# Kernel optimization log

Hardware: AMD Instinct MI355X
Metric: run time of the kernel (lower is better)

Reference implementation:

```python
import jax, jax.numpy as jnp
import numpy as np

N_NODES = 100000
N_EDGES = 1600000
IN_FEATS = 128
N_HIDDEN = 128
N_CLASSES = 40
EPS = 1e-12  # torch F.normalize eps


def _sage_conv(h, src, dst, W_self, b_self, W_neigh, b_neigh, act, norm):
    # mean aggregation over in-neighbors: dst receives from src
    agg = jax.ops.segment_sum(h[src], dst, num_segments=N_NODES)  # [N, D]
    deg = jax.ops.segment_sum(jnp.ones(dst.shape, h.dtype), dst, num_segments=N_NODES)
    h_neigh = agg / jnp.maximum(deg, 1.0)[:, None]
    out = h @ W_self + b_self + h_neigh @ W_neigh + b_neigh
    if act:
        out = jax.nn.relu(out)
    if norm:
        out = out / jnp.maximum(
            jnp.linalg.norm(out, axis=1, keepdims=True), EPS)
    return out


def setup_inputs() -> dict:
    key = jax.random.key(0)
    ks = jax.random.split(key, 16)
    def lin(k, fan_in, fan_out):
        s = 1.0 / np.sqrt(fan_in)
        return jax.random.uniform(k, (fan_in, fan_out), jnp.float32, -s, s)
    inp = {
        "features": jax.random.normal(ks[0], (N_NODES, IN_FEATS), jnp.float32),
        "src": jax.random.randint(ks[1], (N_EDGES,), 0, N_NODES, jnp.int32),
        "dst": jax.random.randint(ks[2], (N_EDGES,), 0, N_NODES, jnp.int32),
        # layer 0: in -> hidden
        "Ws0": lin(ks[3], IN_FEATS, N_HIDDEN), "bs0": jnp.zeros((N_HIDDEN,), jnp.float32),
        "Wn0": lin(ks[4], IN_FEATS, N_HIDDEN), "bn0": jnp.zeros((N_HIDDEN,), jnp.float32),
        # layer 1: hidden -> hidden
        "Ws1": lin(ks[5], N_HIDDEN, N_HIDDEN), "bs1": jnp.zeros((N_HIDDEN,), jnp.float32),
        "Wn1": lin(ks[6], N_HIDDEN, N_HIDDEN), "bn1": jnp.zeros((N_HIDDEN,), jnp.float32),
        # layer 2: hidden -> classes (no activation, no norm)
        "Ws2": lin(ks[7], N_HIDDEN, N_CLASSES), "bs2": jnp.zeros((N_CLASSES,), jnp.float32),
        "Wn2": lin(ks[8], N_HIDDEN, N_CLASSES), "bn2": jnp.zeros((N_CLASSES,), jnp.float32),
    }
    return inp


def reference(features, src, dst,
              Ws0, bs0, Wn0, bn0,
              Ws1, bs1, Wn1, bn1,
              Ws2, bs2, Wn2, bn2):
    h = _sage_conv(features, src, dst, Ws0, bs0, Wn0, bn0, act=True, norm=True)
    h = _sage_conv(h, src, dst, Ws1, bs1, Wn1, bn1, act=True, norm=True)
    out = _sage_conv(h, src, dst, Ws2, bs2, Wn2, bn2, act=False, norm=False)
    return out
```

## Files before the change

kernel.cpp:

```cpp
#include <hip/hip_runtime.h>
#include <hip/hip_bf16.h>

#define N_NODES_C 100000
#define N_EDGES_C 1600000
#define N_BUCK ((N_NODES_C + 255) / 256)
#define BCAP 4608
#define PART_NB 160
#define PART_CHUNK ((N_EDGES_C + PART_NB - 1) / PART_NB)

typedef __attribute__((ext_vector_type(8))) short          short8;
typedef __attribute__((ext_vector_type(4))) float          f32x4;
typedef __attribute__((ext_vector_type(4))) unsigned int   u32x4;
typedef __attribute__((ext_vector_type(4))) unsigned short u16x4;

__device__ inline float load1v(const void* p, size_t i, int bf) {
    return bf ? __bfloat162float(((const __hip_bfloat16*)p)[i])
              : ((const float*)p)[i];
}
__device__ inline unsigned short f2bf(float f) {
    __hip_bfloat16 h = __float2bfloat16(f);
    return *reinterpret_cast<unsigned short*>(&h);
}
__device__ inline float bf_lo(unsigned u) { return __uint_as_float(u << 16); }
__device__ inline float bf_hi(unsigned u) { return __uint_as_float(u & 0xffff0000u); }
__device__ inline void acc8(float* a, u32x4 r) {
    a[0] += bf_lo(r.x); a[1] += bf_hi(r.x);
    a[2] += bf_lo(r.y); a[3] += bf_hi(r.y);
    a[4] += bf_lo(r.z); a[5] += bf_hi(r.z);
    a[6] += bf_lo(r.w); a[7] += bf_hi(r.w);
}

__global__ void detect_init(const void* __restrict__ feats, int* __restrict__ gflag,
                            int* __restrict__ bcur) {
    const unsigned short* u = (const unsigned short*)feats;
    int bad = 0;
    for (int i = threadIdx.x; i < 2048; i += 64) {
        unsigned e = (u[i] >> 7) & 0xFF;
        if (e >= 0xC0) bad++;
    }
#pragma unroll
    for (int off = 32; off > 0; off >>= 1) bad += __shfl_down(bad, off, 64);
    if (threadIdx.x == 0) *gflag = (bad == 0) ? 1 : 0;
    for (int b = threadIdx.x; b < N_BUCK; b += 64) bcur[b] = b * BCAP;
}

__global__ __launch_bounds__(256) void partition2(
        const int* __restrict__ src, const int* __restrict__ dst,
        int* __restrict__ bcur, unsigned* __restrict__ pairs) {
    __shared__ int cnt[N_BUCK];
    __shared__ int lbase[N_BUCK];
    int tid = threadIdx.x;
    int e0 = blockIdx.x * PART_CHUNK;
    int e1 = min(e0 + PART_CHUNK, N_EDGES_C);
    for (int i = tid; i < N_BUCK; i += 256) cnt[i] = 0;
    __syncthreads();
    for (int e = e0 + tid; e < e1; e += 256)
        atomicAdd(&cnt[dst[e] >> 8], 1);
    __syncthreads();
    for (int i = tid; i < N_BUCK; i += 256) {
        int c = cnt[i];
        lbase[i] = c ? atomicAdd(&bcur[i], c) : 0;
        cnt[i] = 0;
    }
    __syncthreads();
    for (int e = e0 + tid; e < e1; e += 256) {
        int s = src[e], d = dst[e];
        int bk = d >> 8;
        int pos = lbase[bk] + atomicAdd(&cnt[bk], 1);
        pairs[pos] = ((unsigned)(d & 255) << 17) | (unsigned)s;
    }
}

__global__ void mkboff_kernel(const int* __restrict__ bcur, int* __restrict__ boff) {
    __shared__ int c[N_BUCK];
    int tid = threadIdx.x;
    for (int i = tid; i < N_BUCK; i += 64) c[i] = bcur[i] - i * BCAP;
    __syncthreads();
    if (tid == 0) {
        int run = 0;
        for (int b = 0; b < N_BUCK; ++b) { int t = c[b]; c[b] = run; run += t; }
        boff[N_BUCK] = run;
    }
    __syncthreads();
    for (int i = tid; i < N_BUCK; i += 64) boff[i] = c[i];
}

__global__ __launch_bounds__(256) void bucket_fill(
        const unsigned* __restrict__ pairs, const int* __restrict__ boff,
        int* __restrict__ csr, int* __restrict__ row_start, int* __restrict__ deg) {
    __shared__ int cnt[256], sd[256], lcur[256];
    int b = blockIdx.x, tid = threadIdx.x;
    int pbase = b * BCAP;
    int base = boff[b], count = boff[b + 1] - base;
    cnt[tid] = 0;
    __syncthreads();
    for (int i = tid; i < count; i += 256)
        atomicAdd(&cnt[pairs[pbase + i] >> 17], 1);
    __syncthreads();
    sd[tid] = cnt[tid];
    __syncthreads();
    for (int st = 1; st < 256; st <<= 1) {
        int t = (tid >= st) ? sd[tid - st] : 0;
        __syncthreads();
        sd[tid] += t;
        __syncthreads();
    }
    int excl = sd[tid] - cnt[tid];
    int node = b * 256 + tid;
    if (node < N_NODES_C) { row_start[node] = base + excl; deg[node] = cnt[tid]; }
    lcur[tid] = excl;
    __syncthreads();
    for (int i = tid; i < count; i += 256) {
        unsigned p = pairs[pbase + i];
        int pos = base + atomicAdd(&lcur[p >> 17], 1);
        csr[pos] = (int)(p & 0x1FFFFu);
    }
}

__global__ void prep_weights(const void* Ws0, const void* bs0, const void* Wn0, const void* bn0,
                             const void* Ws1, const void* bs1, const void* Wn1, const void* bn1,
                             const void* Ws2, const void* bs2, const void* Wn2, const void* bn2,
                             unsigned short* __restrict__ Wt, float* __restrict__ bcat,
                             const int* __restrict__ gflag) {
    int gb = *gflag;
    int n = blockIdx.x;
    int k = threadIdx.x;
    if (n < 128) {
        float v = (k < 128) ? load1v(Ws0, (size_t)k * 128 + n, gb)
                            : load1v(Wn0, (size_t)(k - 128) * 128 + n, gb);
        Wt[(size_t)n * 256 + k] = f2bf(v);
        if (k == 0) bcat[n] = load1v(bs0, n, gb) + load1v(bn0, n, gb);
    } else if (n < 256) {
        int c = n - 128;
        float v = (k < 128) ? load1v(Ws1, (size_t)k * 128 + c, gb)
                            : load1v(Wn1, (size_t)(k - 128) * 128 + c, gb);
        Wt[(size_t)n * 256 + k] = f2bf(v);
        if (k == 0) bcat[n] = load1v(bs1, c, gb) + load1v(bn1, c, gb);
    } else {
        int c = n - 256;
        if (k < 128) {
            float v = (c < 40) ? load1v(Ws2, (size_t)k * 40 + c, gb)
                               : load1v(Wn2, (size_t)k * 40 + (c - 40), gb);
            Wt[65536 + (size_t)c * 128 + k] = f2bf(v);
        }
        if (k == 0) bcat[n] = (c < 40) ? load1v(bs2, c, gb) + load1v(bn2, c, gb) : 0.0f;
    }
}

__global__ void gather_kernel(const void* __restrict__ hsrc, int src_stride,
                              int src_mode, int copy_self,
                              const int* __restrict__ csr,
                              const int* __restrict__ row_start,
                              const int* __restrict__ deg,
                              unsigned short* __restrict__ X,
                              const int* __restrict__ gflag) {
    int node = blockIdx.x * 4 + (threadIdx.x >> 6);
    if (node >= N_NODES_C) return;
    int lane = threadIdx.x & 63;
    int bf = (src_mode == 2) ? *gflag : src_mode;
    int start = row_start[node];
    int d = deg[node];
    const int* cp = csr + start;
    float inv = (d > 0) ? 1.0f / (float)d : 0.0f;

    if (bf) {
        int g = lane >> 4, sub = lane & 15;
        float a[8] = {0,0,0,0,0,0,0,0};
        const unsigned short* hb = (const unsigned short*)hsrc;
        for (int base = 0; base < d; base += 64) {
            int n64 = min(d - base, 64);
            int idxr = cp[base + ((lane < n64) ? lane : 0)];
            int nq = n64 >> 2, rem = n64 & 3;
            int i = 0;
            for (; i + 4 <= nq; i += 4) {
                int nb0 = __shfl(idxr, (i + 0) * 4 + g, 64);
                int nb1 = __shfl(idxr, (i + 1) * 4 + g, 64);
                int nb2 = __shfl(idxr, (i + 2) * 4 + g, 64);
                int nb3 = __shfl(idxr, (i + 3) * 4 + g, 64);
                u32x4 r0 = *(const u32x4*)(hb + (size_t)nb0 * src_stride + sub * 8);
                u32x4 r1 = *(const u32x4*)(hb + (size_t)nb1 * src_stride + sub * 8);
                u32x4 r2 = *(const u32x4*)(hb + (size_t)nb2 * src_stride + sub * 8);
                u32x4 r3 = *(const u32x4*)(hb + (size_t)nb3 * src_stride + sub * 8);
                acc8(a, r0); acc8(a, r1); acc8(a, r2); acc8(a, r3);
            }
            for (; i < nq; ++i) {
                int nb0 = __shfl(idxr, i * 4 + g, 64);
                u32x4 r0 = *(const u32x4*)(hb + (size_t)nb0 * src_stride + sub * 8);
                acc8(a, r0);
            }
            if (rem) {
                int nb = __shfl(idxr, nq * 4 + g, 64);
                if (g < rem) {
                    u32x4 r = *(const u32x4*)(hb + (size_t)nb * src_stride + sub * 8);
                    acc8(a, r);
                }
            }
        }
#pragma unroll
        for (int j = 0; j < 8; ++j) {
            a[j] += __shfl_xor(a[j], 16, 64);
            a[j] += __shfl_xor(a[j], 32, 64);
        }
        if (g == 0) {
            u32x4 o;
            o.x = (unsigned)f2bf(a[0] * inv) | ((unsigned)f2bf(a[1] * inv) << 16);
            o.y = (unsigned)f2bf(a[2] * inv) | ((unsigned)f2bf(a[3] * inv) << 16);
            o.z = (unsigned)f2bf(a[4] * inv) | ((unsigned)f2bf(a[5] * inv) << 16);
            o.w = (unsigned)f2bf(a[6] * inv) | ((unsigned)f2bf(a[7] * inv) << 16);
            *(u32x4*)(X + (size_t)node * 256 + 128 + sub * 8) = o;
        }
        if (copy_self && g == 1) {
            u32x4 raw = *(const u32x4*)(hb + (size_t)node * src_stride + sub * 8);
            *(u32x4*)(X + (size_t)node * 256 + sub * 8) = raw;
        }
    } else {
        int g = lane >> 5, sub = lane & 31;
        float a[4] = {0,0,0,0};
        const float* hf = (const float*)hsrc;
        int nfull = d >> 1, rem = d & 1;
        for (int i = 0; i < nfull; ++i) {
            int nb = cp[i * 2 + g];
            f32x4 raw = *(const f32x4*)(hf + (size_t)nb * src_stride + sub * 4);
            a[0] += raw.x; a[1] += raw.y; a[2] += raw.z; a[3] += raw.w;
        }
        if (g < rem) {
            int nb = cp[nfull * 2 + g];
            f32x4 raw = *(const f32x4*)(hf + (size_t)nb * src_stride + sub * 4);
            a[0] += raw.x; a[1] += raw.y; a[2] += raw.z; a[3] += raw.w;
        }
#pragma unroll
        for (int j = 0; j < 4; ++j) a[j] += __shfl_xor(a[j], 32, 64);
        if (g == 0) {
            u16x4 o = { f2bf(a[0] * inv), f2bf(a[1] * inv), f2bf(a[2] * inv), f2bf(a[3] * inv) };
            *(u16x4*)(X + (size_t)node * 256 + 128 + sub * 4) = o;
        }
        if (copy_self && g == 1) {
            f32x4 raw = *(const f32x4*)(hf + (size_t)node * src_stride + sub * 4);
            u16x4 o = { f2bf(raw.x), f2bf(raw.y), f2bf(raw.z), f2bf(raw.w) };
            *(u16x4*)(X + (size_t)node * 256 + sub * 4) = o;
        }
    }
}

template <int NCT, int KT, int CHK, bool ACTNORM, bool DUAL>
__global__ __launch_bounds__(256) void mfma_gemm(
        const unsigned short* __restrict__ X, int astride,
        const u32x4* __restrict__ Wg,
        const float* __restrict__ bias,
        unsigned short* __restrict__ out, int out_stride,
        unsigned short* __restrict__ Ybuf, unsigned short* __restrict__ Zbuf,
        int n_nodes) {
    __shared__ u32x4 ldsW[NCT * 16 * CHK];
    int tid = threadIdx.x;
    for (int c = tid; c < NCT * 16 * CHK; c += 256) {
        int nrow = c / CHK, ch = c % CHK;
        ldsW[nrow * CHK + (ch ^ (nrow & 7))] = Wg[c];
    }
    __syncthreads();

    int wave = tid >> 6, lane = tid & 63;
    int quad = lane >> 4, sub = lane & 15;
    int mynode = blockIdx.x * 64 + wave * 16 + sub;
    int arow = (mynode < n_nodes) ? mynode : (n_nodes - 1);
    const unsigned short* ap = X + (size_t)arow * astride + quad * 8;

    f32x4 acc[NCT];
#pragma unroll
    for (int ct = 0; ct < NCT; ++ct) acc[ct] = (f32x4){0,0,0,0};

    short8 av = *(const short8*)ap;
#pragma unroll
    for (int kt = 0; kt < KT; ++kt) {
        short8 av_next = av;
        if (kt < KT - 1) av_next = *(const short8*)(ap + (kt + 1) * 32);
        int chunk = kt * 4 + quad;
#pragma unroll
        for (int ct = 0; ct < NCT; ++ct) {
            int ncol = ct * 16 + sub;
            union { u32x4 u; short8 s; } cv;
            cv.u = ldsW[ncol * CHK + (chunk ^ (ncol & 7))];
            acc[ct] = __builtin_amdgcn_mfma_f32_16x16x32_bf16(cv.s, av, acc[ct], 0, 0, 0);
        }
        av = av_next;
    }

    float ss = 0.0f;
#pragma unroll
    for (int ct = 0; ct < NCT; ++ct) {
        f32x4 b4 = *(const f32x4*)(bias + ct * 16 + quad * 4);
#pragma unroll
        for (int r = 0; r < 4; ++r) {
            float v = acc[ct][r] + b4[r];
            if (ACTNORM) { v = fmaxf(v, 0.0f); ss += v * v; }
            acc[ct][r] = v;
        }
    }
    float scale = 1.0f;
    if (ACTNORM) {
        ss += __shfl_xor(ss, 16, 64);
        ss += __shfl_xor(ss, 32, 64);
        scale = 1.0f / fmaxf(sqrtf(ss), 1e-12f);
    }
    if (mynode < n_nodes) {
#pragma unroll
        for (int ct = 0; ct < NCT; ++ct) {
            int c0 = ct * 16 + quad * 4;
            u16x4 o = { f2bf(acc[ct][0] * scale), f2bf(acc[ct][1] * scale),
                        f2bf(acc[ct][2] * scale), f2bf(acc[ct][3] * scale) };
            if (DUAL) {
                if (c0 < 40) *(u16x4*)(Zbuf + (size_t)mynode * 64 + c0) = o;
                else         *(u16x4*)(Ybuf + (size_t)mynode * 64 + (c0 - 40)) = o;
            } else {
                *(u16x4*)(out + (size_t)mynode * out_stride + c0) = o;
            }
        }
    }
}

__global__ void combine_kernel(const unsigned short* __restrict__ Y2,
                               const unsigned short* __restrict__ Z2,
                               const int* __restrict__ csr,
                               const int* __restrict__ row_start,
                               const int* __restrict__ deg,
                               void* __restrict__ out,
                               const int* __restrict__ gflag) {
    int node = blockIdx.x * 4 + (threadIdx.x >> 6);
    if (node >= N_NODES_C) return;
    int lane = threadIdx.x & 63;
    int g = lane >> 3, sub = lane & 7;
    int start = row_start[node], d = deg[node];
    const int* cp = csr + start;
    float a[8] = {0,0,0,0,0,0,0,0};
    int nfull = d >> 3, rem = d & 7;
    int i = 0;
    for (; i + 2 <= nfull; i += 2) {
        int nb0 = cp[i * 8 + g];
        int nb1 = cp[i * 8 + 8 + g];
        u32x4 r0 = *(const u32x4*)(Y2 + (size_t)nb0 * 64 + sub * 8);
        u32x4 r1 = *(const u32x4*)(Y2 + (size_t)nb1 * 64 + sub * 8);
        acc8(a, r0); acc8(a, r1);
    }
    if (i < nfull) {
        int nb = cp[i * 8 + g];
        u32x4 r = *(const u32x4*)(Y2 + (size_t)nb * 64 + sub * 8);
        acc8(a, r);
    }
    if (g < rem) {
        int nb = cp[nfull * 8 + g];
        u32x4 r = *(const u32x4*)(Y2 + (size_t)nb * 64 + sub * 8);
        acc8(a, r);
    }
#pragma unroll
    for (int j = 0; j < 8; ++j) {
        a[j] += __shfl_xor(a[j], 8, 64);
        a[j] += __shfl_xor(a[j], 16, 64);
        a[j] += __shfl_xor(a[j], 32, 64);
    }
    if (g == 0 && sub < 5) {
        float inv = (d > 0) ? 1.0f / (float)d : 0.0f;
        u32x4 z = *(const u32x4*)(Z2 + (size_t)node * 64 + sub * 8);
        float v[8];
        v[0] = a[0] * inv + bf_lo(z.x); v[1] = a[1] * inv + bf_hi(z.x);
        v[2] = a[2] * inv + bf_lo(z.y); v[3] = a[3] * inv + bf_hi(z.y);
        v[4] = a[4] * inv + bf_lo(z.z); v[5] = a[5] * inv + bf_hi(z.z);
        v[6] = a[6] * inv + bf_lo(z.w); v[7] = a[7] * inv + bf_hi(z.w);
        if (*gflag) {
            u32x4 o;
            o.x = (unsigned)f2bf(v[0]) | ((unsigned)f2bf(v[1]) << 16);
            o.y = (unsigned)f2bf(v[2]) | ((unsigned)f2bf(v[3]) << 16);
            o.z = (unsigned)f2bf(v[4]) | ((unsigned)f2bf(v[5]) << 16);
            o.w = (unsigned)f2bf(v[6]) | ((unsigned)f2bf(v[7]) << 16);
            *(u32x4*)((unsigned short*)out + (size_t)node * 40 + sub * 8) = o;
        } else {
            float* op = (float*)out + (size_t)node * 40 + sub * 8;
            f32x4 o0 = { v[0], v[1], v[2], v[3] };
            f32x4 o1 = { v[4], v[5], v[6], v[7] };
            *(f32x4*)op = o0;
            *(f32x4*)(op + 4) = o1;
        }
    }
}

extern "C" void kernel_launch(void* const* d_in, const int* in_sizes, int n_in,
                              void* d_out, int out_size, void* d_ws, size_t ws_size,
                              hipStream_t stream) {
    const void* feats = d_in[0];
    const int*  src   = (const int*)d_in[1];
    const int*  dst   = (const int*)d_in[2];

    char* ws = (char*)d_ws;
    unsigned short* X0   = (unsigned short*)ws;
    unsigned short* X1   = (unsigned short*)(ws + 51200000);
    unsigned short* Wt   = (unsigned short*)(ws + 102400000);
    float*          bcat = (float*)(ws + 102912000);
    unsigned short* Y2   = (unsigned short*)(ws + 102916096);
    unsigned short* Z2   = (unsigned short*)(ws + 115716096);
    unsigned*       pairs= (unsigned*)(ws + 102916096);
    int*  csr       = (int*)(ws + 128516096);
    int*  row_start = (int*)(ws + 134916096);
    int*  deg       = (int*)(ws + 135316096);
    int*  boff      = (int*)(ws + 135718144);
    int*  bcur      = (int*)(ws + 135720192);
    int*  gflag     = (int*)(ws + 135722240);

    detect_init<<<1, 64, 0, stream>>>(feats, gflag, bcur);

    partition2<<<PART_NB, 256, 0, stream>>>(src, dst, bcur, pairs);
    mkboff_kernel<<<1, 64, 0, stream>>>(bcur, boff);
    bucket_fill<<<N_BUCK, 256, 0, stream>>>(pairs, boff, csr, row_start, deg);

    prep_weights<<<336, 256, 0, stream>>>(
        d_in[3], d_in[4], d_in[5], d_in[6],
        d_in[7], d_in[8], d_in[9], d_in[10],
        d_in[11], d_in[12], d_in[13], d_in[14], Wt, bcat, gflag);

    const int gblk = (N_NODES_C + 3) / 4;
    const int mblk = (N_NODES_C + 63) / 64;

    gather_kernel<<<gblk, 256, 0, stream>>>(feats, 128, 2, 1, csr, row_start, deg, X0, gflag);
    mfma_gemm<8, 8, 32, true, false><<<mblk, 256, 0, stream>>>(
        X0, 256, (const u32x4*)Wt, bcat, X1, 256, nullptr, nullptr, N_NODES_C);

    gather_kernel<<<gblk, 256, 0, stream>>>(X1, 256, 1, 0, csr, row_start, deg, X1, gflag);
    mfma_gemm<8, 8, 32, true, false><<<mblk, 256, 0, stream>>>(
        X1, 256, (const u32x4*)(Wt + 128 * 256), bcat + 128, X0, 256, nullptr, nullptr, N_NODES_C);

    mfma_gemm<5, 4, 16, false, true><<<mblk, 256, 0, stream>>>(
        X0, 256, (const u32x4*)(Wt + 65536), bcat + 256, nullptr, 0, Y2, Z2, N_NODES_C);

    combine_kernel<<<gblk, 256, 0, stream>>>(Y2, Z2, csr, row_start, deg, d_out, gflag);
}
```

Baseline: 478.3 us.

## Map one node per 16-lane group in gather and compact layer-2 buffers

```diff
diff --git a/kernel.cpp b/kernel.cpp
--- a/kernel.cpp
+++ b/kernel.cpp
@@ -147,97 +147,132 @@
     }
 }
 
-__global__ void gather_kernel(const void* __restrict__ hsrc, int src_stride,
-                              int src_mode, int copy_self,
-                              const int* __restrict__ csr,
-                              const int* __restrict__ row_start,
-                              const int* __restrict__ deg,
-                              unsigned short* __restrict__ X,
-                              const int* __restrict__ gflag) {
-    int node = blockIdx.x * 4 + (threadIdx.x >> 6);
-    if (node >= N_NODES_C) return;
-    int lane = threadIdx.x & 63;
-    int bf = (src_mode == 2) ? *gflag : src_mode;
-    int start = row_start[node];
-    int d = deg[node];
+__global__ __launch_bounds__(256) void gather_kernel(
+        const void* __restrict__ hsrc, int src_stride,
+        int src_mode, int copy_self,
+        const int* __restrict__ csr,
+        const int* __restrict__ row_start,
+        const int* __restrict__ deg,
+        unsigned short* __restrict__ X,
+        const int* __restrict__ gflag) {
+    int wave = threadIdx.x >> 6, lane = threadIdx.x & 63;
+    int g = lane >> 4, sub = lane & 15;
+    int srcLane = lane & 48;
+    int node = blockIdx.x * 16 + wave * 4 + g;
+    bool valid = node < N_NODES_C;
+    int vnode = valid ? node : (N_NODES_C - 1);
+    int start = row_start[vnode];
+    int d = valid ? deg[vnode] : 0;
     const int* cp = csr + start;
     float inv = (d > 0) ? 1.0f / (float)d : 0.0f;
+    int bf = (src_mode == 2) ? *gflag : src_mode;
 
     if (bf) {
-        int g = lane >> 4, sub = lane & 15;
-        float a[8] = {0,0,0,0,0,0,0,0};
         const unsigned short* hb = (const unsigned short*)hsrc;
-        for (int base = 0; base < d; base += 64) {
-            int n64 = min(d - base, 64);
-            int idxr = cp[base + ((lane < n64) ? lane : 0)];
-            int nq = n64 >> 2, rem = n64 & 3;
+        float a[8] = {0, 0, 0, 0, 0, 0, 0, 0};
+        for (int base = 0; base < d; base += 16) {
+            int n16 = min(d - base, 16);
+            int idxr = cp[base + ((sub < n16) ? sub : 0)];
             int i = 0;
-            for (; i + 4 <= nq; i += 4) {
-                int nb0 = __shfl(idxr, (i + 0) * 4 + g, 64);
-                int nb1 = __shfl(idxr, (i + 1) * 4 + g, 64);
-                int nb2 = __shfl(idxr, (i + 2) * 4 + g, 64);
-                int nb3 = __shfl(idxr, (i + 3) * 4 + g, 64);
+            for (; i + 8 <= n16; i += 8) {
+                int nb0 = __shfl(idxr, srcLane + i + 0, 64);
+                int nb1 = __shfl(idxr, srcLane + i + 1, 64);
+                int nb2 = __shfl(idxr, srcLane + i + 2, 64);
+                int nb3 = __shfl(idxr, srcLane + i + 3, 64);
+                int nb4 = __shfl(idxr, srcLane + i + 4, 64);
+                int nb5 = __shfl(idxr, srcLane + i + 5, 64);
+                int nb6 = __shfl(idxr, srcLane + i + 6, 64);
+                int nb7 = __shfl(idxr, srcLane + i + 7, 64);
+                u32x4 r0 = *(const u32x4*)(hb + (size_t)nb0 * src_stride + sub * 8);
+                u32x4 r1 = *(const u32x4*)(hb + (size_t)nb1 * src_stride + sub * 8);
+                u32x4 r2 = *(const u32x4*)(hb + (size_t)nb2 * src_stride + sub * 8);
+                u32x4 r3 = *(const u32x4*)(hb + (size_t)nb3 * src_stride + sub * 8);
+                u32x4 r4 = *(const u32x4*)(hb + (size_t)nb4 * src_stride + sub * 8);
+                u32x4 r5 = *(const u32x4*)(hb + (size_t)nb5 * src_stride + sub * 8);
+                u32x4 r6 = *(const u32x4*)(hb + (size_t)nb6 * src_stride + sub * 8);
+                u32x4 r7 = *(const u32x4*)(hb + (size_t)nb7 * src_stride + sub * 8);
+                acc8(a, r0); acc8(a, r1); acc8(a, r2); acc8(a, r3);
+                acc8(a, r4); acc8(a, r5); acc8(a, r6); acc8(a, r7);
+            }
+            for (; i + 4 <= n16; i += 4) {
+                int nb0 = __shfl(idxr, srcLane + i + 0, 64);
+                int nb1 = __shfl(idxr, srcLane + i + 1, 64);
+                int nb2 = __shfl(idxr, srcLane + i + 2, 64);
+                int nb3 = __shfl(idxr, srcLane + i + 3, 64);
                 u32x4 r0 = *(const u32x4*)(hb + (size_t)nb0 * src_stride + sub * 8);
                 u32x4 r1 = *(const u32x4*)(hb + (size_t)nb1 * src_stride + sub * 8);
                 u32x4 r2 = *(const u32x4*)(hb + (size_t)nb2 * src_stride + sub * 8);
                 u32x4 r3 = *(const u32x4*)(hb + (size_t)nb3 * src_stride + sub * 8);
                 acc8(a, r0); acc8(a, r1); acc8(a, r2); acc8(a, r3);
             }
-            for (; i < nq; ++i) {
-                int nb0 = __shfl(idxr, i * 4 + g, 64);
-                u32x4 r0 = *(const u32x4*)(hb + (size_t)nb0 * src_stride + sub * 8);
-                acc8(a, r0);
-            }
-            if (rem) {
-                int nb = __shfl(idxr, nq * 4 + g, 64);
-                if (g < rem) {
-                    u32x4 r = *(const u32x4*)(hb + (size_t)nb * src_stride + sub * 8);
-                    acc8(a, r);
-                }
-            }
-        }
-#pragma unroll
-        for (int j = 0; j < 8; ++j) {
-            a[j] += __shfl_xor(a[j], 16, 64);
-            a[j] += __shfl_xor(a[j], 32, 64);
-        }
-        if (g == 0) {
+            for (; i < n16; ++i) {
+                int nb = __shfl(idxr, srcLane + i, 64);
+                u32x4 r = *(const u32x4*)(hb + (size_t)nb * src_stride + sub * 8);
+                acc8(a, r);
+            }
+        }
+        if (valid) {
             u32x4 o;
             o.x = (unsigned)f2bf(a[0] * inv) | ((unsigned)f2bf(a[1] * inv) << 16);
             o.y = (unsigned)f2bf(a[2] * inv) | ((unsigned)f2bf(a[3] * inv) << 16);
             o.z = (unsigned)f2bf(a[4] * inv) | ((unsigned)f2bf(a[5] * inv) << 16);
             o.w = (unsigned)f2bf(a[6] * inv) | ((unsigned)f2bf(a[7] * inv) << 16);
             *(u32x4*)(X + (size_t)node * 256 + 128 + sub * 8) = o;
-        }
-        if (copy_self && g == 1) {
-            u32x4 raw = *(const u32x4*)(hb + (size_t)node * src_stride + sub * 8);
-            *(u32x4*)(X + (size_t)node * 256 + sub * 8) = raw;
+            if (copy_self) {
+                u32x4 raw = *(const u32x4*)(hb + (size_t)node * src_stride + sub * 8);
+                *(u32x4*)(X + (size_t)node * 256 + sub * 8) = raw;
+            }
         }
     } else {
-        int g = lane >> 5, sub = lane & 31;
-        float a[4] = {0,0,0,0};
         const float* hf = (const float*)hsrc;
-        int nfull = d >> 1, rem = d & 1;
-        for (int i = 0; i < nfull; ++i) {
-            int nb = cp[i * 2 + g];
-            f32x4 raw = *(const f32x4*)(hf + (size_t)nb * src_stride + sub * 4);
-            a[0] += raw.x; a[1] += raw.y; a[2] += raw.z; a[3] += raw.w;
-        }
-        if (g < rem) {
-            int nb = cp[nfull * 2 + g];
-            f32x4 raw = *(const f32x4*)(hf + (size_t)nb * src_stride + sub * 4);
-            a[0] += raw.x; a[1] += raw.y; a[2] += raw.z; a[3] += raw.w;
-        }
-#pragma unroll
-        for (int j = 0; j < 4; ++j) a[j] += __shfl_xor(a[j], 32, 64);
-        if (g == 0) {
-            u16x4 o = { f2bf(a[0] * inv), f2bf(a[1] * inv), f2bf(a[2] * inv), f2bf(a[3] * inv) };
-            *(u16x4*)(X + (size_t)node * 256 + 128 + sub * 4) = o;
-        }
-        if (copy_self && g == 1) {
-            f32x4 raw = *(const f32x4*)(hf + (size_t)node * src_stride + sub * 4);
-            u16x4 o = { f2bf(raw.x), f2bf(raw.y), f2bf(raw.z), f2bf(raw.w) };
-            *(u16x4*)(X + (size_t)node * 256 + sub * 4) = o;
+        float a[8] = {0, 0, 0, 0, 0, 0, 0, 0};
+        for (int base = 0; base < d; base += 16) {
+            int n16 = min(d - base, 16);
+            int idxr = cp[base + ((sub < n16) ? sub : 0)];
+            int i = 0;
+            for (; i + 4 <= n16; i += 4) {
+                int nb0 = __shfl(idxr, srcLane + i + 0, 64);
+                int nb1 = __shfl(idxr, srcLane + i + 1, 64);
+                int nb2 = __shfl(idxr, srcLane + i + 2, 64);
+                int nb3 = __shfl(idxr, srcLane + i + 3, 64);
+                const float* p0 = hf + (size_t)nb0 * src_stride + sub * 4;
+                const float* p1 = hf + (size_t)nb1 * src_stride + sub * 4;
+                const float* p2 = hf + (size_t)nb2 * src_stride + sub * 4;
+                const float* p3 = hf + (size_t)nb3 * src_stride + sub * 4;
+                f32x4 a0 = *(const f32x4*)p0, b0 = *(const f32x4*)(p0 + 64);
+                f32x4 a1 = *(const f32x4*)p1, b1 = *(const f32x4*)(p1 + 64);
+                f32x4 a2 = *(const f32x4*)p2, b2 = *(const f32x4*)(p2 + 64);
+                f32x4 a3 = *(const f32x4*)p3, b3 = *(const f32x4*)(p3 + 64);
+#pragma unroll
+                for (int k = 0; k < 4; ++k) {
+                    a[k] += a0[k] + a1[k] + a2[k] + a3[k];
+                    a[4 + k] += b0[k] + b1[k] + b2[k] + b3[k];
+                }
+            }
+            for (; i < n16; ++i) {
+                int nb = __shfl(idxr, srcLane + i, 64);
+                const float* p0 = hf + (size_t)nb * src_stride + sub * 4;
+                f32x4 a0 = *(const f32x4*)p0, b0 = *(const f32x4*)(p0 + 64);
+#pragma unroll
+                for (int k = 0; k < 4; ++k) { a[k] += a0[k]; a[4 + k] += b0[k]; }
+            }
+        }
+        if (valid) {
+            u16x4 oa = { f2bf(a[0] * inv), f2bf(a[1] * inv),
+                         f2bf(a[2] * inv), f2bf(a[3] * inv) };
+            u16x4 ob = { f2bf(a[4] * inv), f2bf(a[5] * inv),
+                         f2bf(a[6] * inv), f2bf(a[7] * inv) };
+            *(u16x4*)(X + (size_t)node * 256 + 128 + sub * 4) = oa;
+            *(u16x4*)(X + (size_t)node * 256 + 128 + 64 + sub * 4) = ob;
+            if (copy_self) {
+                const float* sp = hf + (size_t)node * src_stride + sub * 4;
+                f32x4 ra = *(const f32x4*)sp;
+                f32x4 rb = *(const f32x4*)(sp + 64);
+                u16x4 sa = { f2bf(ra.x), f2bf(ra.y), f2bf(ra.z), f2bf(ra.w) };
+                u16x4 sb = { f2bf(rb.x), f2bf(rb.y), f2bf(rb.z), f2bf(rb.w) };
+                *(u16x4*)(X + (size_t)node * 256 + sub * 4) = sa;
+                *(u16x4*)(X + (size_t)node * 256 + 64 + sub * 4) = sb;
+            }
         }
     }
 }
@@ -308,8 +343,8 @@
             u16x4 o = { f2bf(acc[ct][0] * scale), f2bf(acc[ct][1] * scale),
                         f2bf(acc[ct][2] * scale), f2bf(acc[ct][3] * scale) };
             if (DUAL) {
-                if (c0 < 40) *(u16x4*)(Zbuf + (size_t)mynode * 64 + c0) = o;
-                else         *(u16x4*)(Ybuf + (size_t)mynode * 64 + (c0 - 40)) = o;
+                if (c0 < 40) *(u16x4*)(Zbuf + (size_t)mynode * 40 + c0) = o;
+                else         *(u16x4*)(Ybuf + (size_t)mynode * 40 + (c0 - 40)) = o;
             } else {
                 *(u16x4*)(out + (size_t)mynode * out_stride + c0) = o;
             }
@@ -331,23 +366,24 @@
     int start = row_start[node], d = deg[node];
     const int* cp = csr + start;
     float a[8] = {0,0,0,0,0,0,0,0};
+    int rd = (sub < 5) ? sub : 4;
     int nfull = d >> 3, rem = d & 7;
     int i = 0;
     for (; i + 2 <= nfull; i += 2) {
         int nb0 = cp[i * 8 + g];
         int nb1 = cp[i * 8 + 8 + g];
-        u32x4 r0 = *(const u32x4*)(Y2 + (size_t)nb0 * 64 + sub * 8);
-        u32x4 r1 = *(const u32x4*)(Y2 + (size_t)nb1 * 64 + sub * 8);
+        u32x4 r0 = *(const u32x4*)(Y2 + (size_t)nb0 * 40 + rd * 8);
+        u32x4 r1 = *(const u32x4*)(Y2 + (size_t)nb1 * 40 + rd * 8);
         acc8(a, r0); acc8(a, r1);
     }
     if (i < nfull) {
         int nb = cp[i * 8 + g];
-        u32x4 r = *(const u32x4*)(Y2 + (size_t)nb * 64 + sub * 8);
+        u32x4 r = *(const u32x4*)(Y2 + (size_t)nb * 40 + rd * 8);
         acc8(a, r);
     }
     if (g < rem) {
         int nb = cp[nfull * 8 + g];
-        u32x4 r = *(const u32x4*)(Y2 + (size_t)nb * 64 + sub * 8);
+        u32x4 r = *(const u32x4*)(Y2 + (size_t)nb * 40 + rd * 8);
         acc8(a, r);
     }
 #pragma unroll
@@ -358,7 +394,7 @@
     }
     if (g == 0 && sub < 5) {
         float inv = (d > 0) ? 1.0f / (float)d : 0.0f;
-        u32x4 z = *(const u32x4*)(Z2 + (size_t)node * 64 + sub * 8);
+        u32x4 z = *(const u32x4*)(Z2 + (size_t)node * 40 + sub * 8);
         float v[8];
         v[0] = a[0] * inv + bf_lo(z.x); v[1] = a[1] * inv + bf_hi(z.x);
         v[2] = a[2] * inv + bf_lo(z.y); v[3] = a[3] * inv + bf_hi(z.y);
@@ -414,7 +450,8 @@
         d_in[7], d_in[8], d_in[9], d_in[10],
         d_in[11], d_in[12], d_in[13], d_in[14], Wt, bcat, gflag);
 
-    const int gblk = (N_NODES_C + 3) / 4;
+    const int gblk = (N_NODES_C + 15) / 16;
+    const int cblk = (N_NODES_C + 3) / 4;
     const int mblk = (N_NODES_C + 63) / 64;
 
     gather_kernel<<<gblk, 256, 0, stream>>>(feats, 128, 2, 1, csr, row_start, deg, X0, gflag);
@@ -428,5 +465,5 @@
     mfma_gemm<5, 4, 16, false, true><<<mblk, 256, 0, stream>>>(
         X0, 256, (const u32x4*)(Wt + 65536), bcat + 256, nullptr, 0, Y2, Z2, N_NODES_C);
 
-    combine_kernel<<<gblk, 256, 0, stream>>>(Y2, Z2, csr, row_start, deg, d_out, gflag);
-}
+    combine_kernel<<<cblk, 256, 0, stream>>>(Y2, Z2, csr, row_start, deg, d_out, gflag);
+}
```

Result: faster. 463.4 us (-3.1%).
